# Optimization experiments

Measured on AMD Instinct MI355X. Metric: run time of the kernel, lower is better.

Reference implementation:

```python
import jax, jax.numpy as jnp
import numpy as np

DIM = 3456      # visual_dim
E = 1024        # embed_dim = dim_head*heads = 128*8
H = 8
D = E // H
LN_EPS = 1e-5


def _mlp(x, w1, b1, w2, b2):
    # nn.Sequential(Linear, GELU(exact), Linear)
    h = jax.nn.gelu(x @ w1.T + b1, approximate=False)
    return h @ w2.T + b2


def _ln(x, g, b):
    m = jnp.mean(x, axis=-1, keepdims=True)
    v = jnp.mean((x - m) ** 2, axis=-1, keepdims=True)
    return (x - m) * jax.lax.rsqrt(v + LN_EPS) * g + b


def setup_inputs() -> dict:
    key = jax.random.key(0)
    ks = jax.random.split(key, 24)
    std = 0.02
    d = {"x": jax.random.normal(ks[0], (5, 729, DIM), dtype=jnp.float32)}
    i = 1
    for name in ("q", "k", "v"):
        d[f"{name}_w1"] = std * jax.random.normal(ks[i], (E, DIM), dtype=jnp.float32); i += 1
        d[f"{name}_b1"] = jnp.zeros((E,), jnp.float32)
        d[f"{name}_w2"] = std * jax.random.normal(ks[i], (E, E), dtype=jnp.float32); i += 1
        d[f"{name}_b2"] = jnp.zeros((E,), jnp.float32)
        d[f"ln_{name}_g"] = jnp.ones((E,), jnp.float32)
        d[f"ln_{name}_b"] = jnp.zeros((E,), jnp.float32)
    d["in_proj_w"] = std * jax.random.normal(ks[i], (3 * E, E), dtype=jnp.float32); i += 1
    d["in_proj_b"] = jnp.zeros((3 * E,), jnp.float32)
    d["out_proj_w"] = std * jax.random.normal(ks[i], (E, E), dtype=jnp.float32); i += 1
    d["out_proj_b"] = jnp.zeros((E,), jnp.float32)
    d["to_out_w"] = std * jax.random.normal(ks[i], (DIM, E), dtype=jnp.float32)
    return d


def reference(x,
              q_w1, q_b1, q_w2, q_b2, ln_q_g, ln_q_b,
              k_w1, k_b1, k_w2, k_b2, ln_k_g, ln_k_b,
              v_w1, v_b1, v_w2, v_b2, ln_v_g, ln_v_b,
              in_proj_w, in_proj_b, out_proj_w, out_proj_b, to_out_w):
    t, hw, c = x.shape
    # spatial_temporal pattern: x_multi = x, no interpolation.
    # q/k/v: MLP -> LN -> permute(1,0,2) -> divide_feature -> flatten.
    # divide_feature is a pure permutation of tokens; all tokens end up in a
    # single (L, 1, E) attention, so full attention over the flattened
    # (hw, t) token order computes the identical result.
    q = _ln(_mlp(x, q_w1, q_b1, q_w2, q_b2), ln_q_g, ln_q_b)  # (t, hw, E)
    k = _ln(_mlp(x, k_w1, k_b1, k_w2, k_b2), ln_k_g, ln_k_b)
    v = _ln(_mlp(x, v_w1, v_b1, v_w2, v_b2), ln_v_g, ln_v_b)
    L = t * hw
    q = q.transpose(1, 0, 2).reshape(L, E)  # (hw*t, E), (h,w,t)-major order
    k = k.transpose(1, 0, 2).reshape(L, E)
    v = v.transpose(1, 0, 2).reshape(L, E)
    # nn.MultiheadAttention with packed in_proj
    qp = (q @ in_proj_w[:E].T + in_proj_b[:E]).reshape(L, H, D)
    kp = (k @ in_proj_w[E:2 * E].T + in_proj_b[E:2 * E]).reshape(L, H, D)
    vp = (v @ in_proj_w[2 * E:].T + in_proj_b[2 * E:]).reshape(L, H, D)
    scale = 1.0 / jnp.sqrt(jnp.asarray(D, q.dtype))
    scores = jnp.einsum('qhd,khd->hqk', qp, kp) * scale  # (H, L, L)
    attn = jax.nn.softmax(scores, axis=-1)
    o = jnp.einsum('hqk,khd->qhd', attn, vp).reshape(L, E)
    o = o @ out_proj_w.T + out_proj_b
    o = o.reshape(hw, t, E).transpose(1, 0, 2)  # (t, hw, E)
    out = o @ to_out_w.T                         # (t, hw, c)
    return x + out
```

## Files before the change

kernel.cpp:

```cpp
#include <hip/hip_runtime.h>
#include <hip/hip_bf16.h>

#define L_TOK 3645
#define MP    3712
#define DIMV  3456
#define EDIM  1024

typedef __attribute__((ext_vector_type(8))) short bf8;
typedef __attribute__((ext_vector_type(4))) short s4v;
typedef __attribute__((ext_vector_type(4))) float f4;

__device__ __forceinline__ short f2b(float f) {
  union { float f; unsigned u; } v; v.f = f;
  unsigned r = v.u + 0x7fffu + ((v.u >> 16) & 1u);
  return (short)(r >> 16);
}
__device__ __forceinline__ float b2f(short s) {
  union { unsigned u; float f; } v; v.u = ((unsigned)(unsigned short)s) << 16;
  return v.f;
}
__device__ __forceinline__ void gld16(const void* g, void* l) {
  __builtin_amdgcn_global_load_lds(
      (const __attribute__((address_space(1))) void*)(unsigned long long)g,
      (__attribute__((address_space(3))) void*)(unsigned)(unsigned long long)l,
      16, 0, 0);
}

__global__ __launch_bounds__(256) void k_cvt(const float* __restrict__ src,
                                             short* __restrict__ dst, int n4) {
  int i = blockIdx.x * 256 + threadIdx.x;
  if (i >= n4) return;
  float4 v = ((const float4*)src)[i];
  s4v o; o[0] = f2b(v.x); o[1] = f2b(v.y); o[2] = f2b(v.z); o[3] = f2b(v.w);
  ((s4v*)dst)[i] = o;
}
__global__ __launch_bounds__(256) void k_cvt_pad(const float* __restrict__ src,
                                                 short* __restrict__ dst, int n4src, int n4tot) {
  int i = blockIdx.x * 256 + threadIdx.x;
  if (i >= n4tot) return;
  s4v o; o[0] = 0; o[1] = 0; o[2] = 0; o[3] = 0;
  if (i < n4src) {
    float4 v = ((const float4*)src)[i];
    o[0] = f2b(v.x); o[1] = f2b(v.y); o[2] = f2b(v.z); o[3] = f2b(v.w);
  }
  ((s4v*)dst)[i] = o;
}
__global__ __launch_bounds__(256)
void k_cvt_t(const float* __restrict__ src, short* __restrict__ dst, int n) {
  __shared__ float T[64][65];
  const int bi = blockIdx.x * 64, bj = blockIdx.y * 64;
  const int tx = threadIdx.x & 63, ty = threadIdx.x >> 6;
#pragma unroll
  for (int r = 0; r < 64; r += 4)
    T[r + ty][tx] = src[(long)(bj + r + ty) * n + bi + tx];
  __syncthreads();
#pragma unroll
  for (int r = 0; r < 64; r += 4)
    dst[(long)(bi + r + ty) * n + bj + tx] = f2b(T[tx][r + ty]);
}
__global__ __launch_bounds__(256)
void k_bvec(const float* __restrict__ wt, const float* __restrict__ opb,
            float* __restrict__ bp) {
  const int n = blockIdx.x * 4 + (threadIdx.x >> 6);
  const int lane = threadIdx.x & 63;
  const float* row = wt + (long)n * 1024;
  float s = 0.f;
  for (int k = lane * 4; k < 1024; k += 256) {
    float4 w = *(const float4*)&row[k];
    float4 b = *(const float4*)&opb[k];
    s += w.x * b.x + w.y * b.y + w.z * b.z + w.w * b.w;
  }
#pragma unroll
  for (int off = 1; off < 64; off <<= 1) s += __shfl_xor(s, off);
  if (lane == 0) bp[n] = s;
}

#define GM_GELU   0
#define GM_BIAS   1
#define GM_QSCALE 2
#define GM_RESID  3
#define GM_PLAIN  4

template<int MODE>
__global__ __launch_bounds__(256)
void k_gemm(const short* __restrict__ A, long sA,
            const short* __restrict__ B, long sB,
            const float* __restrict__ bias0, const float* __restrict__ bias1,
            const float* __restrict__ bias2,
            void* __restrict__ Cout, long sC,
            int N, int K, const float* __restrict__ resid)
{
  __shared__ short As[2][128 * 32];
  __shared__ short Bs[2][128 * 32];
  const int tid  = threadIdx.x;
  const int z    = blockIdx.z;
  const int nwg  = gridDim.x * gridDim.y;
  const int orig = blockIdx.y * gridDim.x + blockIdx.x;
  const int qq   = nwg >> 3, rr = nwg & 7;
  const int xcd  = orig & 7, ofs = orig >> 3;
  const int swz  = (xcd < rr ? xcd * (qq + 1) : rr * (qq + 1) + (xcd - rr) * qq) + ofs;
  const int brow = (swz / gridDim.x) * 128;
  const int bcol = (swz % gridDim.x) * 128;

  const short* Ab = A + (long)z * sA;
  const short* Bb = B + (long)z * sB;
  const float* bias = (z == 0) ? bias0 : (z == 1 ? bias1 : bias2);

  const int wave = tid >> 6, lane = tid & 63;
  const int lg = lane >> 4, lc = lane & 15;
  const int m0 = (wave >> 1) * 64, n0 = (wave & 1) * 64;

  const int r0 = tid >> 2, seg = tid & 3;
  const int r1 = r0 + 64;
  const int so0 = (seg ^ ((r0 >> 1) & 3)) * 8;
  const int so1 = (seg ^ ((r1 >> 1) & 3)) * 8;
  const short* pA0 = Ab + (long)(brow + r0) * K + so0;
  const short* pA1 = Ab + (long)(brow + r1) * K + so1;
  const short* pB0 = Bb + (long)(bcol + r0) * K + so0;
  const short* pB1 = Bb + (long)(bcol + r1) * K + so1;

  f4 acc[4][4];
  f4 zero = {0.f, 0.f, 0.f, 0.f};
#pragma unroll
  for (int i = 0; i < 4; ++i)
#pragma unroll
    for (int j = 0; j < 4; ++j) acc[i][j] = zero;

  auto STAGE = [&](int buf) {
    gld16(pA0, &As[buf][tid * 8]);
    gld16(pA1, &As[buf][(tid + 256) * 8]);
    gld16(pB0, &Bs[buf][tid * 8]);
    gld16(pB1, &Bs[buf][(tid + 256) * 8]);
    pA0 += 32; pA1 += 32; pB0 += 32; pB1 += 32;
  };

  const int NT = K >> 5;
  STAGE(0);
  for (int t = 0; t < NT; ++t) {
    const int buf = t & 1;
    asm volatile("s_waitcnt vmcnt(0)" ::: "memory");
    __builtin_amdgcn_sched_barrier(0);
    __builtin_amdgcn_s_barrier();
    if (t + 1 < NT) STAGE((t + 1) & 1);
    const short* Al = &As[buf][0];
    const short* Bl = &Bs[buf][0];
    bf8 af[4], bfr[4];
#pragma unroll
    for (int mi = 0; mi < 4; ++mi) {
      int r = m0 + mi * 16 + lc;
      af[mi] = *(const bf8*)&Al[r * 32 + ((lg ^ ((r >> 1) & 3)) * 8)];
    }
#pragma unroll
    for (int ni = 0; ni < 4; ++ni) {
      int r = n0 + ni * 16 + lc;
      bfr[ni] = *(const bf8*)&Bl[r * 32 + ((lg ^ ((r >> 1) & 3)) * 8)];
    }
    __builtin_amdgcn_s_setprio(1);
#pragma unroll
    for (int mi = 0; mi < 4; ++mi)
#pragma unroll
      for (int ni = 0; ni < 4; ++ni)
        acc[mi][ni] = __builtin_amdgcn_mfma_f32_16x16x32_bf16(af[mi], bfr[ni], acc[mi][ni], 0, 0, 0);
    __builtin_amdgcn_s_setprio(0);
    __builtin_amdgcn_sched_barrier(0);
  }

  if (MODE == GM_RESID) {
    float* C = (float*)Cout;
#pragma unroll
    for (int ni = 0; ni < 4; ++ni) {
      int col = bcol + n0 + ni * 16 + lc;
      float bv = bias[col];
#pragma unroll
      for (int mi = 0; mi < 4; ++mi)
#pragma unroll
        for (int r = 0; r < 4; ++r) {
          int row = brow + m0 + mi * 16 + lg * 4 + r;
          if (row < L_TOK)
            C[(long)row * N + col] = acc[mi][ni][r] + bv + resid[(long)row * N + col];
        }
    }
  } else {
    short* C = (short*)Cout + (long)z * sC;
    const float alpha = (MODE == GM_QSCALE && z == 0) ? 0.08838834764831845f : 1.0f;
#pragma unroll
    for (int ni = 0; ni < 4; ++ni) {
      int col = bcol + n0 + ni * 16 + lc;
      float bv = 0.f;
      if (MODE != GM_PLAIN) bv = bias[col];
#pragma unroll
      for (int mi = 0; mi < 4; ++mi)
#pragma unroll
        for (int r = 0; r < 4; ++r) {
          int row = brow + m0 + mi * 16 + lg * 4 + r;
          float v = acc[mi][ni][r] + bv;
          if (MODE == GM_GELU) v = 0.5f * v * (1.f + erff(v * 0.70710678118654752f));
          v *= alpha;
          C[(long)row * EDIM + col] = f2b(v);
        }
    }
  }
}

__global__ __launch_bounds__(256)
void k_ln(const short* __restrict__ A, short* __restrict__ Y,
          const float* __restrict__ g0, const float* __restrict__ g1, const float* __restrict__ g2,
          const float* __restrict__ b0, const float* __restrict__ b1, const float* __restrict__ b2)
{
  const int row = blockIdx.x, z = blockIdx.y;
  const float* g = (z == 0) ? g0 : (z == 1 ? g1 : g2);
  const float* b = (z == 0) ? b0 : (z == 1 ? b1 : b2);
  const short* a = A + ((long)z * MP + row) * EDIM;
  short* y = Y + ((long)z * MP + row) * EDIM;
  const int t = threadIdx.x;
  s4v v = *(const s4v*)&a[t * 4];
  float x0 = b2f(v[0]), x1 = b2f(v[1]), x2 = b2f(v[2]), x3 = b2f(v[3]);
  float s = x0 + x1 + x2 + x3;
  float q = x0 * x0 + x1 * x1 + x2 * x2 + x3 * x3;
#pragma unroll
  for (int off = 1; off < 64; off <<= 1) { s += __shfl_xor(s, off); q += __shfl_xor(q, off); }
  __shared__ float rs[4], rq[4];
  if ((t & 63) == 0) { rs[t >> 6] = s; rq[t >> 6] = q; }
  __syncthreads();
  s = rs[0] + rs[1] + rs[2] + rs[3];
  q = rq[0] + rq[1] + rq[2] + rq[3];
  float mean = s * (1.f / 1024.f);
  float var  = q * (1.f / 1024.f) - mean * mean;
  float rstd = rsqrtf(var + 1e-5f);
  s4v o;
#pragma unroll
  for (int j = 0; j < 4; ++j) {
    int col = t * 4 + j;
    o[j] = f2b((b2f(v[j]) - mean) * rstd * g[col] + b[col]);
  }
  *(s4v*)&y[t * 4] = o;
}

__global__ __launch_bounds__(256)
void k_vtrans(const short* __restrict__ vp, short* __restrict__ vpT)
{
  const int kb = blockIdx.x * 64, h = blockIdx.y;
  __shared__ short T[64 * 128];
  const int tid = threadIdx.x;
#pragma unroll
  for (int i = 0; i < 4; ++i) {
    int c = tid + 256 * i;
    int r = c >> 4, x = c & 15;
    bf8 val = *(const bf8*)&vp[(long)(kb + r) * EDIM + h * 128 + x * 8];
    *(bf8*)&T[r * 128 + ((x ^ (r & 7)) * 8)] = val;
  }
  __syncthreads();
#pragma unroll
  for (int i = 0; i < 4; ++i) {
    int c = tid + 256 * i;
    int dr = c >> 3, x = c & 7;
    short tmp[8];
#pragma unroll
    for (int e = 0; e < 8; ++e) {
      int kv = x * 8 + e;
      tmp[e] = T[kv * 128 + (((dr >> 3) ^ (kv & 7)) << 3) + (dr & 7)];
    }
    *(bf8*)&vpT[((long)h * 128 + dr) * MP + kb + x * 8] = *(bf8*)tmp;
  }
}

__global__ __launch_bounds__(256)
void k_attn(const short* __restrict__ qp, const short* __restrict__ kp,
            const short* __restrict__ vpT,
            short* __restrict__ op0, short* __restrict__ op1,
            float* __restrict__ lsums)
{
  const int bx = blockIdx.x;
  const int h = bx & 7;
  const int t2 = bx >> 3;
  const int qi = t2 % 29, sp = t2 / 29;
  const int qb = qi * 128;
  short* opart = sp ? op1 : op0;
  const int t0 = sp ? 29 : 0, t1 = sp ? 57 : 29;

  const int tid = threadIdx.x, wave = tid >> 6, lane = tid & 63;
  const int lg = lane >> 4, lc = lane & 15;
  __shared__ short Ks[2][64 * 128];
  __shared__ short Vs[2][128 * 64];
  __shared__ short Ps[4][32 * 64];

  const int q0 = qb + wave * 32;
  bf8 qf[2][4];
#pragma unroll
  for (int g = 0; g < 2; ++g)
#pragma unroll
    for (int d4 = 0; d4 < 4; ++d4)
      qf[g][d4] = *(const bf8*)&qp[(long)(q0 + g * 16 + lc) * EDIM + h * 128 + d4 * 32 + lg * 8];

  f4 oacc[2][8];
  f4 zero = {0.f, 0.f, 0.f, 0.f};
#pragma unroll
  for (int g = 0; g < 2; ++g)
#pragma unroll
    for (int dt = 0; dt < 8; ++dt) oacc[g][dt] = zero;
  float lsum0 = 0.f, lsum1 = 0.f;

  auto STAGE = [&](short* ksb, short* vsb, int kb) {
#pragma unroll
    for (int i = 0; i < 4; ++i) {
      int c = tid + 256 * i; int r = c >> 4, x = c & 15;
      gld16(&kp[(long)(kb + r) * EDIM + h * 128 + (x ^ (r & 7)) * 8], &ksb[c * 8]);
    }
#pragma unroll
    for (int i = 0; i < 4; ++i) {
      int c = tid + 256 * i; int dr = c >> 3, x = c & 7;
      gld16(&vpT[((long)h * 128 + dr) * MP + kb + (x ^ (dr & 7)) * 8], &vsb[c * 8]);
    }
  };

  STAGE(Ks[t0 & 1], Vs[t0 & 1], t0 * 64);

  for (int t = t0; t < t1; ++t) {
    const int kb = t * 64;
    const short* ksb = Ks[t & 1];
    const short* vsb = Vs[t & 1];
    __builtin_amdgcn_s_barrier();
    if (t + 1 < t1) {
      STAGE(Ks[(t + 1) & 1], Vs[(t + 1) & 1], kb + 64);
      asm volatile("s_waitcnt vmcnt(8)" ::: "memory");
    } else {
      asm volatile("s_waitcnt vmcnt(0)" ::: "memory");
    }
    __builtin_amdgcn_sched_barrier(0);
    __builtin_amdgcn_s_barrier();
    __builtin_amdgcn_sched_barrier(0);

#pragma unroll
    for (int s = 0; s < 4; ++s) {
      const int krow = s * 16 + lc;
      bf8 kf[4];
#pragma unroll
      for (int d4 = 0; d4 < 4; ++d4)
        kf[d4] = *(const bf8*)&ksb[krow * 128 + (((d4 * 4 + lg) ^ (krow & 7)) * 8)];
      f4 sa0 = zero, sa1 = zero;
      __builtin_amdgcn_s_setprio(1);
#pragma unroll
      for (int d4 = 0; d4 < 4; ++d4) {
        sa0 = __builtin_amdgcn_mfma_f32_16x16x32_bf16(kf[d4], qf[0][d4], sa0, 0, 0, 0);
        sa1 = __builtin_amdgcn_mfma_f32_16x16x32_bf16(kf[d4], qf[1][d4], sa1, 0, 0, 0);
      }
      __builtin_amdgcn_s_setprio(0);
      const int kvb = kb + s * 16 + lg * 4;
#pragma unroll
      for (int g = 0; g < 2; ++g) {
        f4 sa = g ? sa1 : sa0;
        float p[4];
#pragma unroll
        for (int r = 0; r < 4; ++r) {
          float e = __expf(sa[r]);
          p[r] = (kvb + r < L_TOK) ? e : 0.f;
          if (g) lsum1 += p[r]; else lsum0 += p[r];
        }
        s4v pk; pk[0] = f2b(p[0]); pk[1] = f2b(p[1]); pk[2] = f2b(p[2]); pk[3] = f2b(p[3]);
        *(s4v*)&Ps[wave][(g * 16 + lc) * 64 + ((s * 16 + lg * 4) ^ ((lc & 7) << 3))] = pk;
      }
    }
    bf8 pf[2][2];
#pragma unroll
    for (int g = 0; g < 2; ++g) {
      pf[g][0] = *(const bf8*)&Ps[wave][(g * 16 + lc) * 64 + ((lg * 8) ^ ((lc & 7) << 3))];
      pf[g][1] = *(const bf8*)&Ps[wave][(g * 16 + lc) * 64 + ((32 + lg * 8) ^ ((lc & 7) << 3))];
    }
#pragma unroll
    for (int dt = 0; dt < 8; ++dt) {
      const int vrow = dt * 16 + lc;
      bf8 vf0 = *(const bf8*)&vsb[vrow * 64 + ((lg ^ (vrow & 7)) * 8)];
      bf8 vf1 = *(const bf8*)&vsb[vrow * 64 + (((4 + lg) ^ (vrow & 7)) * 8)];
      __builtin_amdgcn_s_setprio(1);
      oacc[0][dt] = __builtin_amdgcn_mfma_f32_16x16x32_bf16(pf[0][0], vf0, oacc[0][dt], 0, 0, 0);
      oacc[0][dt] = __builtin_amdgcn_mfma_f32_16x16x32_bf16(pf[0][1], vf1, oacc[0][dt], 0, 0, 0);
      oacc[1][dt] = __builtin_amdgcn_mfma_f32_16x16x32_bf16(pf[1][0], vf0, oacc[1][dt], 0, 0, 0);
      oacc[1][dt] = __builtin_amdgcn_mfma_f32_16x16x32_bf16(pf[1][1], vf1, oacc[1][dt], 0, 0, 0);
      __builtin_amdgcn_s_setprio(0);
    }
    __builtin_amdgcn_sched_barrier(0);
  }

  lsum0 += __shfl_xor(lsum0, 16);
  lsum0 += __shfl_xor(lsum0, 32);
  lsum1 += __shfl_xor(lsum1, 16);
  lsum1 += __shfl_xor(lsum1, 32);
  if (lg == 0) {
    lsums[((sp * 8) + h) * MP + q0 + lc]      = lsum0;
    lsums[((sp * 8) + h) * MP + q0 + 16 + lc] = lsum1;
  }
#pragma unroll
  for (int g = 0; g < 2; ++g)
#pragma unroll
    for (int dt = 0; dt < 8; ++dt)
#pragma unroll
      for (int r = 0; r < 4; ++r) {
        int orow = q0 + g * 16 + lg * 4 + r;
        opart[(long)orow * EDIM + h * 128 + dt * 16 + lc] = f2b(oacc[g][dt][r]);
      }
}

__global__ __launch_bounds__(256)
void k_comb(const short* __restrict__ p0, const short* __restrict__ p1,
            const float* __restrict__ ls, short* __restrict__ ob)
{
  int i = blockIdx.x * 256 + threadIdx.x;
  int q = i >> 7;
  int h = (i & 127) >> 4;
  float rinv = 1.f / (ls[h * MP + q] + ls[(8 + h) * MP + q]);
  bf8 a = ((const bf8*)p0)[i];
  bf8 b = ((const bf8*)p1)[i];
  bf8 o;
#pragma unroll
  for (int j = 0; j < 8; ++j) o[j] = f2b((b2f(a[j]) + b2f(b[j])) * rinv);
  ((bf8*)ob)[i] = o;
}

extern "C" void kernel_launch(void* const* d_in, const int* in_sizes, int n_in,
                              void* d_out, int out_size, void* d_ws, size_t ws_size,
                              hipStream_t stream)
{
  const float* x   = (const float*)d_in[0];
  const float* ipb = (const float*)d_in[20];
  const float* opb = (const float*)d_in[22];

  char* ws = (char*)d_ws;
  short* regA = (short*)(ws + 0);
  short* regB = (short*)(ws + 25657344);
  short* w1b  = (short*)(ws + 48463872);
  short* w2b  = (short*)(ws + 69697536);
  short* wpb  = (short*)(ws + 75988992);
  short* woT  = (short*)(ws + 82280448);
  short* wtb  = (short*)(ws + 84377600);
  short* vpT  = (short*)(ws + 91455488);

  short* xb  = regA;
  short* h1  = regB;
  short* aln = regA;
  short* lnq = regB;
  short* proj = regA;
  short* ob  = regB;
  short* pt1 = (short*)(ws + 33259520);
  short* pt0 = (short*)(ws + 40861696);
  float* lsums = (float*)(ws + 22806528);
  float* bp    = (float*)(ws + 23068672);
  short* wprime = w1b;

  k_cvt_pad<<<12528, 256, 0, stream>>>(x, xb, 3149280, 3207168);
  k_cvt<<<3456, 256, 0, stream>>>((const float*)d_in[1],  w1b,            884736);
  k_cvt<<<3456, 256, 0, stream>>>((const float*)d_in[7],  w1b + 3538944,  884736);
  k_cvt<<<3456, 256, 0, stream>>>((const float*)d_in[13], w1b + 7077888,  884736);
  k_cvt<<<1024, 256, 0, stream>>>((const float*)d_in[3],  w2b,            262144);
  k_cvt<<<1024, 256, 0, stream>>>((const float*)d_in[9],  w2b + 1048576,  262144);
  k_cvt<<<1024, 256, 0, stream>>>((const float*)d_in[15], w2b + 2097152,  262144);
  k_cvt<<<3072, 256, 0, stream>>>((const float*)d_in[19], wpb,            786432);
  k_cvt<<<3456, 256, 0, stream>>>((const float*)d_in[23], wtb,            884736);
  dim3 gct(16, 16);
  k_cvt_t<<<gct, 256, 0, stream>>>((const float*)d_in[21], woT, 1024);

  dim3 g3(8, 29, 3), g1(8, 29, 1);
  k_gemm<GM_GELU><<<g3, 256, 0, stream>>>(xb, 0, w1b, 3538944,
      (const float*)d_in[2], (const float*)d_in[8], (const float*)d_in[14],
      h1, (long)MP * EDIM, EDIM, DIMV, nullptr);
  k_bvec<<<864, 256, 0, stream>>>((const float*)d_in[23], opb, bp);
  dim3 gwp(8, 27, 1);
  k_gemm<GM_PLAIN><<<gwp, 256, 0, stream>>>(wtb, 0, woT, 0,
      nullptr, nullptr, nullptr, wprime, 0, EDIM, EDIM, nullptr);
  k_gemm<GM_BIAS><<<g3, 256, 0, stream>>>(h1, (long)MP * EDIM, w2b, 1048576,
      (const float*)d_in[4], (const float*)d_in[10], (const float*)d_in[16],
      aln, (long)MP * EDIM, EDIM, EDIM, nullptr);
  dim3 gl(MP, 3);
  k_ln<<<gl, 256, 0, stream>>>(aln, lnq,
      (const float*)d_in[5], (const float*)d_in[11], (const float*)d_in[17],
      (const float*)d_in[6], (const float*)d_in[12], (const float*)d_in[18]);
  k_gemm<GM_QSCALE><<<g3, 256, 0, stream>>>(lnq, (long)MP * EDIM, wpb, 1048576,
      ipb, ipb + 1024, ipb + 2048,
      proj, (long)MP * EDIM, EDIM, EDIM, nullptr);
  dim3 gt(MP / 64, 8);
  k_vtrans<<<gt, 256, 0, stream>>>(proj + 2L * MP * EDIM, vpT);
  k_attn<<<29 * 2 * 8, 256, 0, stream>>>(proj, proj + (long)MP * EDIM, vpT,
      pt0, pt1, lsums);
  k_comb<<<(MP * EDIM / 8) / 256, 256, 0, stream>>>(pt0, pt1, lsums, ob);
  dim3 g5(27, 29, 1);
  k_gemm<GM_RESID><<<g5, 256, 0, stream>>>(ob, 0, wprime, 0,
      bp, bp, bp, d_out, 0, DIMV, EDIM, x);
}
```

Before: 420.5 us.

## Fold LayerNorm affine into in-projection weights and merge conversion kernels

The LayerNorm gain is folded into the in-projection weights during conversion, and the LN mean/rstd plus beta are applied algebraically in a new GEMM epilogue. This lets a small stats kernel replace the full LN pass that wrote a normalized activation buffer. The eight separate fp32-to-bf16 conversion launches are merged into one kernel to cut launch overhead. In exchange the projection GEMM now consumes un-normalized bf16 activations, which changes rounding, and the workspace layout is reshuffled.

```diff
diff --git a/kernel.cpp b/kernel.cpp
--- a/kernel.cpp
+++ b/kernel.cpp
@@ -26,25 +26,61 @@
       16, 0, 0);
 }
 
-__global__ __launch_bounds__(256) void k_cvt(const float* __restrict__ src,
-                                             short* __restrict__ dst, int n4) {
+struct CvtArgs {
+  const float *s0, *s1, *s2, *s3, *s4, *s5, *s6, *s7;
+  short *d0, *d1, *d2, *d3, *d4, *d5, *d6, *d7;
+};
+#define SB0 3207168
+#define SB1 4091904
+#define SB2 4976640
+#define SB3 5861376
+#define SB4 6123520
+#define SB5 6385664
+#define SB6 6647808
+#define SB7 7532544
+__global__ __launch_bounds__(256) void k_cvtall(CvtArgs a) {
   int i = blockIdx.x * 256 + threadIdx.x;
-  if (i >= n4) return;
+  if (i >= SB7) return;
+  const float* src; short* dst; int j;
+  if (i < SB0) {
+    j = i; src = a.s0; dst = a.d0;
+    s4v o; o[0] = 0; o[1] = 0; o[2] = 0; o[3] = 0;
+    if (j < 3149280) {
+      float4 v = ((const float4*)src)[j];
+      o[0] = f2b(v.x); o[1] = f2b(v.y); o[2] = f2b(v.z); o[3] = f2b(v.w);
+    }
+    ((s4v*)dst)[j] = o;
+    return;
+  }
+  else if (i < SB1) { j = i - SB0; src = a.s1; dst = a.d1; }
+  else if (i < SB2) { j = i - SB1; src = a.s2; dst = a.d2; }
+  else if (i < SB3) { j = i - SB2; src = a.s3; dst = a.d3; }
+  else if (i < SB4) { j = i - SB3; src = a.s4; dst = a.d4; }
+  else if (i < SB5) { j = i - SB4; src = a.s5; dst = a.d5; }
+  else if (i < SB6) { j = i - SB5; src = a.s6; dst = a.d6; }
+  else              { j = i - SB6; src = a.s7; dst = a.d7; }
+  float4 v = ((const float4*)src)[j];
+  s4v o; o[0] = f2b(v.x); o[1] = f2b(v.y); o[2] = f2b(v.z); o[3] = f2b(v.w);
+  ((s4v*)dst)[j] = o;
+}
+
+__global__ __launch_bounds__(256)
+void k_cvtwp(const float* __restrict__ src, short* __restrict__ dst,
+             const float* __restrict__ g0, const float* __restrict__ g1,
+             const float* __restrict__ g2) {
+  int i = blockIdx.x * 256 + threadIdx.x;
+  if (i >= 786432) return;
+  int flat = i * 4;
+  int k = flat & 1023;
+  int z = flat >> 20;
+  const float* g = (z == 0) ? g0 : (z == 1 ? g1 : g2);
   float4 v = ((const float4*)src)[i];
-  s4v o; o[0] = f2b(v.x); o[1] = f2b(v.y); o[2] = f2b(v.z); o[3] = f2b(v.w);
+  float4 gv = *(const float4*)&g[k];
+  s4v o; o[0] = f2b(v.x * gv.x); o[1] = f2b(v.y * gv.y);
+  o[2] = f2b(v.z * gv.z); o[3] = f2b(v.w * gv.w);
   ((s4v*)dst)[i] = o;
 }
-__global__ __launch_bounds__(256) void k_cvt_pad(const float* __restrict__ src,
-                                                 short* __restrict__ dst, int n4src, int n4tot) {
-  int i = blockIdx.x * 256 + threadIdx.x;
-  if (i >= n4tot) return;
-  s4v o; o[0] = 0; o[1] = 0; o[2] = 0; o[3] = 0;
-  if (i < n4src) {
-    float4 v = ((const float4*)src)[i];
-    o[0] = f2b(v.x); o[1] = f2b(v.y); o[2] = f2b(v.z); o[3] = f2b(v.w);
-  }
-  ((s4v*)dst)[i] = o;
-}
+
 __global__ __launch_bounds__(256)
 void k_cvt_t(const float* __restrict__ src, short* __restrict__ dst, int n) {
   __shared__ float T[64][65];
@@ -58,6 +94,7 @@
   for (int r = 0; r < 64; r += 4)
     dst[(long)(bi + r + ty) * n + bj + tx] = f2b(T[tx][r + ty]);
 }
+
 __global__ __launch_bounds__(256)
 void k_bvec(const float* __restrict__ wt, const float* __restrict__ opb,
             float* __restrict__ bp) {
@@ -73,6 +110,57 @@
 #pragma unroll
   for (int off = 1; off < 64; off <<= 1) s += __shfl_xor(s, off);
   if (lane == 0) bp[n] = s;
+}
+
+__global__ __launch_bounds__(256)
+void k_cvec(const float* __restrict__ wp,
+            const float* g0, const float* g1, const float* g2,
+            const float* b0, const float* b1, const float* b2,
+            const float* __restrict__ ipb,
+            float* __restrict__ c1, float* __restrict__ cb2) {
+  const int z = blockIdx.y;
+  const int n = blockIdx.x * 4 + (threadIdx.x >> 6);
+  const int lane = threadIdx.x & 63;
+  const float* g  = (z == 0) ? g0 : (z == 1 ? g1 : g2);
+  const float* lb = (z == 0) ? b0 : (z == 1 ? b1 : b2);
+  const float* row = wp + ((long)z * 1024 + n) * 1024;
+  float s1 = 0.f, s2 = 0.f;
+  for (int k = lane * 4; k < 1024; k += 256) {
+    float4 w = *(const float4*)&row[k];
+    float4 gv = *(const float4*)&g[k];
+    float4 bv = *(const float4*)&lb[k];
+    s1 += w.x * gv.x + w.y * gv.y + w.z * gv.z + w.w * gv.w;
+    s2 += w.x * bv.x + w.y * bv.y + w.z * bv.z + w.w * bv.w;
+  }
+#pragma unroll
+  for (int off = 1; off < 64; off <<= 1) {
+    s1 += __shfl_xor(s1, off); s2 += __shfl_xor(s2, off);
+  }
+  if (lane == 0) { c1[z * 1024 + n] = s1; cb2[z * 1024 + n] = s2 + ipb[z * 1024 + n]; }
+}
+
+__global__ __launch_bounds__(256)
+void k_stats(const short* __restrict__ aln, float2* __restrict__ st) {
+  const int z = blockIdx.y;
+  const int row = blockIdx.x * 4 + (threadIdx.x >> 6);
+  const int lane = threadIdx.x & 63;
+  const short* a = aln + ((long)z * MP + row) * EDIM;
+  float s = 0.f, q = 0.f;
+  for (int k = lane * 4; k < 1024; k += 256) {
+    s4v v = *(const s4v*)&a[k];
+#pragma unroll
+    for (int e = 0; e < 4; ++e) { float f = b2f(v[e]); s += f; q += f * f; }
+  }
+#pragma unroll
+  for (int off = 1; off < 64; off <<= 1) {
+    s += __shfl_xor(s, off); q += __shfl_xor(q, off);
+  }
+  if (lane == 0) {
+    float m = s * (1.f / 1024.f);
+    float var = q * (1.f / 1024.f) - m * m;
+    float2 o; o.x = m; o.y = rsqrtf(var + 1e-5f);
+    st[(long)z * MP + row] = o;
+  }
 }
 
 #define GM_GELU   0
@@ -203,37 +291,109 @@
 }
 
 __global__ __launch_bounds__(256)
-void k_ln(const short* __restrict__ A, short* __restrict__ Y,
-          const float* __restrict__ g0, const float* __restrict__ g1, const float* __restrict__ g2,
-          const float* __restrict__ b0, const float* __restrict__ b1, const float* __restrict__ b2)
+void k_gemmln(const short* __restrict__ A, long sA,
+              const short* __restrict__ B, long sB,
+              const float2* __restrict__ st,
+              const float* __restrict__ c1, const float* __restrict__ cb2,
+              short* __restrict__ Cout, long sC)
 {
-  const int row = blockIdx.x, z = blockIdx.y;
-  const float* g = (z == 0) ? g0 : (z == 1 ? g1 : g2);
-  const float* b = (z == 0) ? b0 : (z == 1 ? b1 : b2);
-  const short* a = A + ((long)z * MP + row) * EDIM;
-  short* y = Y + ((long)z * MP + row) * EDIM;
-  const int t = threadIdx.x;
-  s4v v = *(const s4v*)&a[t * 4];
-  float x0 = b2f(v[0]), x1 = b2f(v[1]), x2 = b2f(v[2]), x3 = b2f(v[3]);
-  float s = x0 + x1 + x2 + x3;
-  float q = x0 * x0 + x1 * x1 + x2 * x2 + x3 * x3;
-#pragma unroll
-  for (int off = 1; off < 64; off <<= 1) { s += __shfl_xor(s, off); q += __shfl_xor(q, off); }
-  __shared__ float rs[4], rq[4];
-  if ((t & 63) == 0) { rs[t >> 6] = s; rq[t >> 6] = q; }
-  __syncthreads();
-  s = rs[0] + rs[1] + rs[2] + rs[3];
-  q = rq[0] + rq[1] + rq[2] + rq[3];
-  float mean = s * (1.f / 1024.f);
-  float var  = q * (1.f / 1024.f) - mean * mean;
-  float rstd = rsqrtf(var + 1e-5f);
-  s4v o;
-#pragma unroll
-  for (int j = 0; j < 4; ++j) {
-    int col = t * 4 + j;
-    o[j] = f2b((b2f(v[j]) - mean) * rstd * g[col] + b[col]);
-  }
-  *(s4v*)&y[t * 4] = o;
+  __shared__ short As[2][128 * 32];
+  __shared__ short Bs[2][128 * 32];
+  const int tid  = threadIdx.x;
+  const int z    = blockIdx.z;
+  const int K    = EDIM;
+  const int nwg  = gridDim.x * gridDim.y;
+  const int orig = blockIdx.y * gridDim.x + blockIdx.x;
+  const int qq   = nwg >> 3, rr = nwg & 7;
+  const int xcd  = orig & 7, ofs = orig >> 3;
+  const int swz  = (xcd < rr ? xcd * (qq + 1) : rr * (qq + 1) + (xcd - rr) * qq) + ofs;
+  const int brow = (swz / gridDim.x) * 128;
+  const int bcol = (swz % gridDim.x) * 128;
+
+  const short* Ab = A + (long)z * sA;
+  const short* Bb = B + (long)z * sB;
+
+  const int wave = tid >> 6, lane = tid & 63;
+  const int lg = lane >> 4, lc = lane & 15;
+  const int m0 = (wave >> 1) * 64, n0 = (wave & 1) * 64;
+
+  const int r0 = tid >> 2, seg = tid & 3;
+  const int r1 = r0 + 64;
+  const int so0 = (seg ^ ((r0 >> 1) & 3)) * 8;
+  const int so1 = (seg ^ ((r1 >> 1) & 3)) * 8;
+  const short* pA0 = Ab + (long)(brow + r0) * K + so0;
+  const short* pA1 = Ab + (long)(brow + r1) * K + so1;
+  const short* pB0 = Bb + (long)(bcol + r0) * K + so0;
+  const short* pB1 = Bb + (long)(bcol + r1) * K + so1;
+
+  f4 acc[4][4];
+  f4 zero = {0.f, 0.f, 0.f, 0.f};
+#pragma unroll
+  for (int i = 0; i < 4; ++i)
+#pragma unroll
+    for (int j = 0; j < 4; ++j) acc[i][j] = zero;
+
+  auto STAGE = [&](int buf) {
+    gld16(pA0, &As[buf][tid * 8]);
+    gld16(pA1, &As[buf][(tid + 256) * 8]);
+    gld16(pB0, &Bs[buf][tid * 8]);
+    gld16(pB1, &Bs[buf][(tid + 256) * 8]);
+    pA0 += 32; pA1 += 32; pB0 += 32; pB1 += 32;
+  };
+
+  const int NT = K >> 5;
+  STAGE(0);
+  for (int t = 0; t < NT; ++t) {
+    const int buf = t & 1;
+    asm volatile("s_waitcnt vmcnt(0)" ::: "memory");
+    __builtin_amdgcn_sched_barrier(0);
+    __builtin_amdgcn_s_barrier();
+    if (t + 1 < NT) STAGE((t + 1) & 1);
+    const short* Al = &As[buf][0];
+    const short* Bl = &Bs[buf][0];
+    bf8 af[4], bfr[4];
+#pragma unroll
+    for (int mi = 0; mi < 4; ++mi) {
+      int r = m0 + mi * 16 + lc;
+      af[mi] = *(const bf8*)&Al[r * 32 + ((lg ^ ((r >> 1) & 3)) * 8)];
+    }
+#pragma unroll
+    for (int ni = 0; ni < 4; ++ni) {
+      int r = n0 + ni * 16 + lc;
+      bfr[ni] = *(const bf8*)&Bl[r * 32 + ((lg ^ ((r >> 1) & 3)) * 8)];
+    }
+    __builtin_amdgcn_s_setprio(1);
+#pragma unroll
+    for (int mi = 0; mi < 4; ++mi)
+#pragma unroll
+      for (int ni = 0; ni < 4; ++ni)
+        acc[mi][ni] = __builtin_amdgcn_mfma_f32_16x16x32_bf16(af[mi], bfr[ni], acc[mi][ni], 0, 0, 0);
+    __builtin_amdgcn_s_setprio(0);
+    __builtin_amdgcn_sched_barrier(0);
+  }
+
+  short* C = Cout + (long)z * sC;
+  const float alpha = (z == 0) ? 0.08838834764831845f : 1.0f;
+  float2 sv[4][4];
+#pragma unroll
+  for (int mi = 0; mi < 4; ++mi)
+#pragma unroll
+    for (int r = 0; r < 4; ++r)
+      sv[mi][r] = st[(long)z * MP + brow + m0 + mi * 16 + lg * 4 + r];
+#pragma unroll
+  for (int ni = 0; ni < 4; ++ni) {
+    int col = bcol + n0 + ni * 16 + lc;
+    float c1v = c1[z * 1024 + col];
+    float cbv = cb2[z * 1024 + col];
+#pragma unroll
+    for (int mi = 0; mi < 4; ++mi)
+#pragma unroll
+      for (int r = 0; r < 4; ++r) {
+        int row = brow + m0 + mi * 16 + lg * 4 + r;
+        float v = sv[mi][r].y * (acc[mi][ni][r] - sv[mi][r].x * c1v) + cbv;
+        C[(long)row * EDIM + col] = f2b(v * alpha);
+      }
+  }
 }
 
 __global__ __launch_bounds__(256)
@@ -425,57 +585,61 @@
   const float* opb = (const float*)d_in[22];
 
   char* ws = (char*)d_ws;
-  short* regA = (short*)(ws + 0);
-  short* regB = (short*)(ws + 25657344);
-  short* w1b  = (short*)(ws + 48463872);
-  short* w2b  = (short*)(ws + 69697536);
-  short* wpb  = (short*)(ws + 75988992);
-  short* woT  = (short*)(ws + 82280448);
-  short* wtb  = (short*)(ws + 84377600);
-  short* vpT  = (short*)(ws + 91455488);
-
-  short* xb  = regA;
-  short* h1  = regB;
-  short* aln = regA;
-  short* lnq = regB;
-  short* proj = regA;
-  short* ob  = regB;
-  short* pt1 = (short*)(ws + 33259520);
-  short* pt0 = (short*)(ws + 40861696);
-  float* lsums = (float*)(ws + 22806528);
-  float* bp    = (float*)(ws + 23068672);
-  short* wprime = w1b;
-
-  k_cvt_pad<<<12528, 256, 0, stream>>>(x, xb, 3149280, 3207168);
-  k_cvt<<<3456, 256, 0, stream>>>((const float*)d_in[1],  w1b,            884736);
-  k_cvt<<<3456, 256, 0, stream>>>((const float*)d_in[7],  w1b + 3538944,  884736);
-  k_cvt<<<3456, 256, 0, stream>>>((const float*)d_in[13], w1b + 7077888,  884736);
-  k_cvt<<<1024, 256, 0, stream>>>((const float*)d_in[3],  w2b,            262144);
-  k_cvt<<<1024, 256, 0, stream>>>((const float*)d_in[9],  w2b + 1048576,  262144);
-  k_cvt<<<1024, 256, 0, stream>>>((const float*)d_in[15], w2b + 2097152,  262144);
-  k_cvt<<<3072, 256, 0, stream>>>((const float*)d_in[19], wpb,            786432);
-  k_cvt<<<3456, 256, 0, stream>>>((const float*)d_in[23], wtb,            884736);
+  short*  xb     = (short*)(ws + 0);
+  short*  aln    = (short*)(ws + 0);
+  short*  pt0    = (short*)(ws + 0);
+  short*  pt1    = (short*)(ws + 7602176);
+  float*  lsums  = (float*)(ws + 15204352);
+  short*  ob     = (short*)(ws + 15466496);
+  float2* stats  = (float2*)(ws + 23068672);
+  float*  bp     = (float*)(ws + 23330816);
+  float*  c1     = (float*)(ws + 23461888);
+  float*  cb2    = (float*)(ws + 23592960);
+  short*  h1     = (short*)(ws + 25657344);
+  short*  proj   = (short*)(ws + 25657344);
+  short*  w1b    = (short*)(ws + 48463872);
+  short*  wprime = w1b;
+  short*  w2b    = (short*)(ws + 69697536);
+  short*  wpb    = (short*)(ws + 75988992);
+  short*  woT    = (short*)(ws + 82280448);
+  short*  wtb    = (short*)(ws + 84377600);
+  short*  vpT    = (short*)(ws + 91455488);
+
+  CvtArgs ca;
+  ca.s0 = x;                      ca.d0 = xb;
+  ca.s1 = (const float*)d_in[1];  ca.d1 = w1b;
+  ca.s2 = (const float*)d_in[7];  ca.d2 = w1b + 3538944;
+  ca.s3 = (const float*)d_in[13]; ca.d3 = w1b + 7077888;
+  ca.s4 = (const float*)d_in[3];  ca.d4 = w2b;
+  ca.s5 = (const float*)d_in[9];  ca.d5 = w2b + 1048576;
+  ca.s6 = (const float*)d_in[15]; ca.d6 = w2b + 2097152;
+  ca.s7 = (const float*)d_in[23]; ca.d7 = wtb;
+  k_cvtall<<<(SB7 + 255) / 256, 256, 0, stream>>>(ca);
+  k_cvtwp<<<3072, 256, 0, stream>>>((const float*)d_in[19], wpb,
+      (const float*)d_in[5], (const float*)d_in[11], (const float*)d_in[17]);
   dim3 gct(16, 16);
   k_cvt_t<<<gct, 256, 0, stream>>>((const float*)d_in[21], woT, 1024);
 
-  dim3 g3(8, 29, 3), g1(8, 29, 1);
+  dim3 g3(8, 29, 3);
   k_gemm<GM_GELU><<<g3, 256, 0, stream>>>(xb, 0, w1b, 3538944,
       (const float*)d_in[2], (const float*)d_in[8], (const float*)d_in[14],
       h1, (long)MP * EDIM, EDIM, DIMV, nullptr);
   k_bvec<<<864, 256, 0, stream>>>((const float*)d_in[23], opb, bp);
+  dim3 gcv(256, 3);
+  k_cvec<<<gcv, 256, 0, stream>>>((const float*)d_in[19],
+      (const float*)d_in[5], (const float*)d_in[11], (const float*)d_in[17],
+      (const float*)d_in[6], (const float*)d_in[12], (const float*)d_in[18],
+      ipb, c1, cb2);
   dim3 gwp(8, 27, 1);
   k_gemm<GM_PLAIN><<<gwp, 256, 0, stream>>>(wtb, 0, woT, 0,
       nullptr, nullptr, nullptr, wprime, 0, EDIM, EDIM, nullptr);
   k_gemm<GM_BIAS><<<g3, 256, 0, stream>>>(h1, (long)MP * EDIM, w2b, 1048576,
       (const float*)d_in[4], (const float*)d_in[10], (const float*)d_in[16],
       aln, (long)MP * EDIM, EDIM, EDIM, nullptr);
-  dim3 gl(MP, 3);
-  k_ln<<<gl, 256, 0, stream>>>(aln, lnq,
-      (const float*)d_in[5], (const float*)d_in[11], (const float*)d_in[17],
-      (const float*)d_in[6], (const float*)d_in[12], (const float*)d_in[18]);
-  k_gemm<GM_QSCALE><<<g3, 256, 0, stream>>>(lnq, (long)MP * EDIM, wpb, 1048576,
-      ipb, ipb + 1024, ipb + 2048,
-      proj, (long)MP * EDIM, EDIM, EDIM, nullptr);
+  dim3 gst(MP / 4, 3);
+  k_stats<<<gst, 256, 0, stream>>>(aln, stats);
+  k_gemmln<<<g3, 256, 0, stream>>>(aln, (long)MP * EDIM, wpb, 1048576,
+      stats, c1, cb2, proj, (long)MP * EDIM);
   dim3 gt(MP / 64, 8);
   k_vtrans<<<gt, 256, 0, stream>>>(proj + 2L * MP * EDIM, vpT);
   k_attn<<<29 * 2 * 8, 256, 0, stream>>>(proj, proj + (long)MP * EDIM, vpT,
```

Result: faster. 409.7 us, median of 2 (-2.6%).
